# Kernel optimization log

Hardware: AMD Instinct MI355X
Metric: run time of the kernel (lower is better)

Reference implementation:

```python
import jax, jax.numpy as jnp
import numpy as np

N, L, D = 8192, 50, 64          # batch nodes, history length, embed_dim
NUM_ITEMS, NUM_ATTRS, NUM_FAM = 50000, 100000, 100000


def setup_inputs() -> dict:
    key = jax.random.key(0)
    ks = jax.random.split(key, 12)
    scale = 0.05
    return {
        "nodes": jax.random.randint(ks[0], (N,), 0, NUM_ITEMS),
        "history_va": jax.random.randint(ks[1], (N, L), 0, NUM_ATTRS),
        "history_af": jax.random.randint(ks[2], (N, L), 0, NUM_FAM),
        "v2e_w": jax.random.normal(ks[3], (NUM_ITEMS, D), jnp.float32) * scale,
        "a2e_w": jax.random.normal(ks[4], (NUM_ATTRS, D), jnp.float32) * scale,
        "f2e_w": jax.random.normal(ks[5], (NUM_FAM, D), jnp.float32) * scale,
        "W1": jax.random.normal(ks[6], (3 * D, D), jnp.float32) * scale,
        "b1": jnp.zeros((D,), jnp.float32),
        "W2": jax.random.normal(ks[7], (D, D), jnp.float32) * scale,
        "b2": jnp.zeros((D,), jnp.float32),
        "w3": jax.random.normal(ks[8], (D, 1), jnp.float32) * scale,
        "b3": jnp.zeros((1,), jnp.float32),
    }


def reference(nodes, history_va, history_af, v2e_w, a2e_w, f2e_w,
              W1, b1, W2, b2, w3, b3):
    # Batched form of the per-node loop (va=True branch).
    e_va = a2e_w[history_va]                       # [N, L, D] gathered attr embeds
    e_af = f2e_w[history_af]                       # [N, L, D] gathered famous embeds
    va_rep = v2e_w[nodes]                          # [N, D]    target item embed
    rep = jnp.broadcast_to(va_rep[:, None, :], e_va.shape)
    x = jnp.concatenate([e_va, rep, e_af], axis=-1)  # [N, L, 3D]
    h = jax.nn.relu(x @ W1 + b1)                   # [N, L, D]
    h = jax.nn.relu(h @ W2 + b2)                   # [N, L, D]
    scores = (h @ w3 + b3)[..., 0]                 # [N, L]
    att = jax.nn.softmax(scores, axis=1)           # softmax over history dim
    # e_va.T @ att per node  ==  weighted sum over history
    return jnp.einsum("nld,nl->nd", e_va, att)     # [N, D]
```

## Files before the change

kernel.cpp:

```cpp
#include <hip/hip_runtime.h>
#include <hip/hip_bf16.h>

typedef __bf16 bf16x8 __attribute__((ext_vector_type(8)));
typedef __bf16 bf16x4 __attribute__((ext_vector_type(4)));
typedef float  f32x4  __attribute__((ext_vector_type(4)));

#define HL   50
#define DD   64
#define NPB  2
#define MR   112
#define MT   7
#define XSS  136

__global__ __launch_bounds__(256) void va_prep_kernel(
    const float* __restrict__ W1, const float* __restrict__ W2,
    const float* __restrict__ w3, const float* __restrict__ b1,
    const float* __restrict__ b2,
    __bf16* __restrict__ wf, float* __restrict__ wsc)
{
    const int tid  = threadIdx.x;
    const int quad = tid >> 6;
    const int col  = tid & 63;
    __bf16* dst = wf + tid * 64;
    #pragma unroll
    for (int t = 0; t < 4; ++t)
        #pragma unroll
        for (int j = 0; j < 8; ++j) {
            int keff = t * 32 + quad * 8 + j;
            int krow = (keff < 64) ? keff : keff + 64;
            dst[t * 8 + j] = (__bf16)W1[krow * 64 + col];
        }
    #pragma unroll
    for (int t = 0; t < 2; ++t)
        #pragma unroll
        for (int j = 0; j < 8; ++j) {
            dst[32 + t * 8 + j] = (__bf16)W1[(64 + t * 32 + quad * 8 + j) * 64 + col];
            dst[48 + t * 8 + j] = (__bf16)W2[(t * 32 + quad * 8 + j) * 64 + col];
        }
    if (tid < 64) {
        wsc[tid]       = w3[tid];
        wsc[64 + tid]  = b1[tid];
        wsc[128 + tid] = b2[tid];
    }
}

__global__ __launch_bounds__(256, 5) void va_agg_kernel(
    const int*    __restrict__ nodes,
    const int*    __restrict__ hva,
    const int*    __restrict__ haf,
    const float*  __restrict__ v2e,
    const float*  __restrict__ a2e,
    const float*  __restrict__ f2e,
    const __bf16* __restrict__ wf,
    const float*  __restrict__ wsc,
    float*        __restrict__ out)
{
    __shared__ __bf16 xs[MR * XSS];
    __shared__ float  pbuf[4 * MR];

    const int tid  = threadIdx.x;
    const int w    = tid >> 6;
    const int lane = tid & 63;
    const int lq   = lane & 15;
    const int quad = lane >> 4;
    const int col  = w * 16 + lq;
    const int n0   = blockIdx.x * NPB;

    {
        const int* hb = hva + n0 * HL;
        const int* fb = haf + n0 * HL;
        #pragma unroll
        for (int i = 0; i < 13; ++i) {
            int t = i * 256 + tid;
            if (t < NPB * HL * 2 * 16) {
                int r = t >> 4, q = t & 15;
                bool va = (r < NPB * HL);
                int gr = va ? r : r - NPB * HL;
                int idx = va ? hb[gr] : fb[gr];
                const float* src = (va ? a2e : f2e) + (size_t)idx * DD + q * 4;
                float4 v = *(const float4*)src;
                bf16x4 pk = {(__bf16)v.x, (__bf16)v.y, (__bf16)v.z, (__bf16)v.w};
                *(bf16x4*)&xs[gr * XSS + (va ? 0 : DD) + q * 4] = pk;
            }
        }
    }

    bf16x8 repf[2];
    #pragma unroll
    for (int t = 0; t < 2; ++t)
        #pragma unroll
        for (int j = 0; j < 8; ++j) repf[t][j] = (__bf16)0.f;
    if (lq < NPB) {
        int nd = nodes[n0 + lq];
        const float* rp = v2e + (size_t)nd * DD;
        #pragma unroll
        for (int t = 0; t < 2; ++t) {
            float4 v0 = *(const float4*)(rp + t * 32 + quad * 8);
            float4 v1 = *(const float4*)(rp + t * 32 + quad * 8 + 4);
            repf[t] = (bf16x8){(__bf16)v0.x, (__bf16)v0.y, (__bf16)v0.z, (__bf16)v0.w,
                               (__bf16)v1.x, (__bf16)v1.y, (__bf16)v1.z, (__bf16)v1.w};
        }
    }

    const __bf16* fbp = wf + (size_t)(quad * 64 + col) * 64;
    bf16x8 b1f[4], b1u[2], b2f[2];
    #pragma unroll
    for (int t = 0; t < 4; ++t) b1f[t] = *(const bf16x8*)(fbp + t * 8);
    #pragma unroll
    for (int t = 0; t < 2; ++t) {
        b1u[t] = *(const bf16x8*)(fbp + 32 + t * 8);
        b2f[t] = *(const bf16x8*)(fbp + 48 + t * 8);
    }
    const float w3c = wsc[col];
    const float b1c = wsc[64 + col];
    const float b2c = wsc[128 + col];

    f32x4 rb = {0.f, 0.f, 0.f, 0.f};
    #pragma unroll
    for (int t = 0; t < 2; ++t)
        rb = __builtin_amdgcn_mfma_f32_16x16x32_bf16(repf[t], b1u[t], rb, 0, 0, 0);
    const float bias0 = __shfl(rb[0], lq) + b1c;
    const float bias1 = __shfl(rb[1], lq) + b1c;

    __syncthreads();

    f32x4 acc[MT];
    #pragma unroll
    for (int mt = 0; mt < MT; ++mt)
        #pragma unroll
        for (int r = 0; r < 4; ++r) {
            int gr = mt * 16 + quad * 4 + r;
            acc[mt][r] = (gr >= HL) ? bias1 : bias0;
        }
    #pragma unroll
    for (int t = 0; t < 4; ++t)
        #pragma unroll
        for (int mt = 0; mt < MT; ++mt) {
            bf16x8 a = *(const bf16x8*)&xs[(mt * 16 + lq) * XSS + t * 32 + quad * 8];
            acc[mt] = __builtin_amdgcn_mfma_f32_16x16x32_bf16(a, b1f[t], acc[mt], 0, 0, 0);
        }
    __syncthreads();
    #pragma unroll
    for (int mt = 0; mt < MT; ++mt)
        #pragma unroll
        for (int r = 0; r < 4; ++r) {
            int gr = mt * 16 + quad * 4 + r;
            xs[gr * XSS + DD + col] = (__bf16)fmaxf(acc[mt][r], 0.f);
        }
    __syncthreads();

    f32x4 a2[MT];
    #pragma unroll
    for (int mt = 0; mt < MT; ++mt) a2[mt] = (f32x4){b2c, b2c, b2c, b2c};
    #pragma unroll
    for (int t = 0; t < 2; ++t)
        #pragma unroll
        for (int mt = 0; mt < MT; ++mt) {
            bf16x8 a = *(const bf16x8*)&xs[(mt * 16 + lq) * XSS + DD + t * 32 + quad * 8];
            a2[mt] = __builtin_amdgcn_mfma_f32_16x16x32_bf16(a, b2f[t], a2[mt], 0, 0, 0);
        }
    #pragma unroll
    for (int mt = 0; mt < MT; ++mt) {
        float p0 = fmaxf(a2[mt][0], 0.f) * w3c;
        float p1 = fmaxf(a2[mt][1], 0.f) * w3c;
        float p2 = fmaxf(a2[mt][2], 0.f) * w3c;
        float p3 = fmaxf(a2[mt][3], 0.f) * w3c;
        #pragma unroll
        for (int m = 1; m < 16; m <<= 1) {
            p0 += __shfl_xor(p0, m);
            p1 += __shfl_xor(p1, m);
            p2 += __shfl_xor(p2, m);
            p3 += __shfl_xor(p3, m);
        }
        if (lq == 0) {
            int rowb = mt * 16 + quad * 4;
            pbuf[w * MR + rowb + 0] = p0;
            pbuf[w * MR + rowb + 1] = p1;
            pbuf[w * MR + rowb + 2] = p2;
            pbuf[w * MR + rowb + 3] = p3;
        }
    }
    __syncthreads();

    const int n  = w & 1;
    const int lh = w >> 1;
    float att;
    {
        float s = -3.0e38f;
        if (lane < HL) {
            int gr = n * HL + lane;
            s = pbuf[gr] + pbuf[MR + gr] + pbuf[2 * MR + gr] + pbuf[3 * MR + gr];
        }
        float mx = s;
        #pragma unroll
        for (int m = 1; m < 64; m <<= 1) mx = fmaxf(mx, __shfl_xor(mx, m));
        float e = (lane < HL) ? __expf(s - mx) : 0.f;
        float sm = e;
        #pragma unroll
        for (int m = 1; m < 64; m <<= 1) sm += __shfl_xor(sm, m);
        att = e / sm;
    }

    {
        float o = 0.f;
        const int lb = lh * 25;
        #pragma unroll
        for (int i = 0; i < 25; ++i) {
            int l = lb + i;
            float av = __shfl(att, l);
            o = fmaf(av, (float)xs[(n * HL + l) * XSS + lane], o);
        }
        float* op = (float*)&xs[(100 + w) * XSS + DD];
        op[lane] = o;
    }
    __syncthreads();
    if (w < NPB) {
        const float* p0 = (const float*)&xs[(100 + w) * XSS + DD];
        const float* p1 = (const float*)&xs[(100 + w + 2) * XSS + DD];
        out[(size_t)(n0 + w) * DD + lane] = p0[lane] + p1[lane];
    }
}

extern "C" void kernel_launch(void* const* d_in, const int* in_sizes, int n_in,
                              void* d_out, int out_size, void* d_ws, size_t ws_size,
                              hipStream_t stream) {
    const int*   nodes = (const int*)d_in[0];
    const int*   hva   = (const int*)d_in[1];
    const int*   haf   = (const int*)d_in[2];
    const float* v2e   = (const float*)d_in[3];
    const float* a2e   = (const float*)d_in[4];
    const float* f2e   = (const float*)d_in[5];
    const float* W1    = (const float*)d_in[6];
    const float* b1    = (const float*)d_in[7];
    const float* W2    = (const float*)d_in[8];
    const float* b2    = (const float*)d_in[9];
    const float* w3    = (const float*)d_in[10];
    float* out = (float*)d_out;

    __bf16* wf  = (__bf16*)d_ws;
    float*  wsc = (float*)((char*)d_ws + 256 * 64 * 2);

    va_prep_kernel<<<1, 256, 0, stream>>>(W1, W2, w3, b1, b2, wf, wsc);

    const int N = in_sizes[0];
    const int blocks = N / NPB;
    va_agg_kernel<<<blocks, 256, 0, stream>>>(nodes, hva, haf, v2e, a2e, f2e,
                                              wf, wsc, out);
}
```

Measured before the change: 167.5 us.

## Process one node per block with 64-row tiles to cut padding waste

Each block now handles a single node, so it works on 50 real rows padded to 64 (4 MFMA row tiles) instead of 100 padded to 112 (7 tiles). Shared memory per block drops, and the launch bound is raised to 8 blocks per CU to increase occupancy. The final weighted sum is split across the 4 waves by interleaved history rows and reduced through shared memory. The cost is twice as many blocks, with the per-block weight fragment loads and setup repeated for each node, plus a larger share of padded rows (14 of 64 versus 12 of 112).

```diff
diff --git a/kernel.cpp b/kernel.cpp
--- a/kernel.cpp
+++ b/kernel.cpp
@@ -7,9 +7,8 @@
 
 #define HL   50
 #define DD   64
-#define NPB  2
-#define MR   112
-#define MT   7
+#define MR   64
+#define MT   4
 #define XSS  136
 
 __global__ __launch_bounds__(256) void va_prep_kernel(
@@ -44,7 +43,7 @@
     }
 }
 
-__global__ __launch_bounds__(256, 5) void va_agg_kernel(
+__global__ __launch_bounds__(256, 8) void va_agg_kernel(
     const int*    __restrict__ nodes,
     const int*    __restrict__ hva,
     const int*    __restrict__ haf,
@@ -64,18 +63,18 @@
     const int lq   = lane & 15;
     const int quad = lane >> 4;
     const int col  = w * 16 + lq;
-    const int n0   = blockIdx.x * NPB;
+    const int node = blockIdx.x;
 
     {
-        const int* hb = hva + n0 * HL;
-        const int* fb = haf + n0 * HL;
-        #pragma unroll
-        for (int i = 0; i < 13; ++i) {
+        const int* hb = hva + node * HL;
+        const int* fb = haf + node * HL;
+        #pragma unroll
+        for (int i = 0; i < 7; ++i) {
             int t = i * 256 + tid;
-            if (t < NPB * HL * 2 * 16) {
+            if (t < HL * 2 * 16) {
                 int r = t >> 4, q = t & 15;
-                bool va = (r < NPB * HL);
-                int gr = va ? r : r - NPB * HL;
+                bool va = (r < HL);
+                int gr = va ? r : r - HL;
                 int idx = va ? hb[gr] : fb[gr];
                 const float* src = (va ? a2e : f2e) + (size_t)idx * DD + q * 4;
                 float4 v = *(const float4*)src;
@@ -90,8 +89,8 @@
     for (int t = 0; t < 2; ++t)
         #pragma unroll
         for (int j = 0; j < 8; ++j) repf[t][j] = (__bf16)0.f;
-    if (lq < NPB) {
-        int nd = nodes[n0 + lq];
+    if (lq == 0) {
+        int nd = nodes[node];
         const float* rp = v2e + (size_t)nd * DD;
         #pragma unroll
         for (int t = 0; t < 2; ++t) {
@@ -120,18 +119,12 @@
     for (int t = 0; t < 2; ++t)
         rb = __builtin_amdgcn_mfma_f32_16x16x32_bf16(repf[t], b1u[t], rb, 0, 0, 0);
     const float bias0 = __shfl(rb[0], lq) + b1c;
-    const float bias1 = __shfl(rb[1], lq) + b1c;
 
     __syncthreads();
 
     f32x4 acc[MT];
     #pragma unroll
-    for (int mt = 0; mt < MT; ++mt)
-        #pragma unroll
-        for (int r = 0; r < 4; ++r) {
-            int gr = mt * 16 + quad * 4 + r;
-            acc[mt][r] = (gr >= HL) ? bias1 : bias0;
-        }
+    for (int mt = 0; mt < MT; ++mt) acc[mt] = (f32x4){bias0, bias0, bias0, bias0};
     #pragma unroll
     for (int t = 0; t < 4; ++t)
         #pragma unroll
@@ -182,15 +175,11 @@
     }
     __syncthreads();
 
-    const int n  = w & 1;
-    const int lh = w >> 1;
     float att;
     {
         float s = -3.0e38f;
-        if (lane < HL) {
-            int gr = n * HL + lane;
-            s = pbuf[gr] + pbuf[MR + gr] + pbuf[2 * MR + gr] + pbuf[3 * MR + gr];
-        }
+        if (lane < HL)
+            s = pbuf[lane] + pbuf[MR + lane] + pbuf[2 * MR + lane] + pbuf[3 * MR + lane];
         float mx = s;
         #pragma unroll
         for (int m = 1; m < 64; m <<= 1) mx = fmaxf(mx, __shfl_xor(mx, m));
@@ -203,21 +192,24 @@
 
     {
         float o = 0.f;
-        const int lb = lh * 25;
-        #pragma unroll
-        for (int i = 0; i < 25; ++i) {
-            int l = lb + i;
-            float av = __shfl(att, l);
-            o = fmaf(av, (float)xs[(n * HL + l) * XSS + lane], o);
-        }
-        float* op = (float*)&xs[(100 + w) * XSS + DD];
+        #pragma unroll
+        for (int i = 0; i < 13; ++i) {
+            int l = w + 4 * i;
+            if (l < HL) {
+                float av = __shfl(att, l);
+                o = fmaf(av, (float)xs[l * XSS + lane], o);
+            }
+        }
+        float* op = (float*)&xs[(50 + 2 * w) * XSS];
         op[lane] = o;
     }
     __syncthreads();
-    if (w < NPB) {
-        const float* p0 = (const float*)&xs[(100 + w) * XSS + DD];
-        const float* p1 = (const float*)&xs[(100 + w + 2) * XSS + DD];
-        out[(size_t)(n0 + w) * DD + lane] = p0[lane] + p1[lane];
+    if (w == 0) {
+        float o = 0.f;
+        #pragma unroll
+        for (int k = 0; k < 4; ++k)
+            o += ((const float*)&xs[(50 + 2 * k) * XSS])[lane];
+        out[(size_t)node * DD + lane] = o;
     }
 }
 
@@ -243,7 +235,6 @@
     va_prep_kernel<<<1, 256, 0, stream>>>(W1, W2, w3, b1, b2, wf, wsc);
 
     const int N = in_sizes[0];
-    const int blocks = N / NPB;
-    va_agg_kernel<<<blocks, 256, 0, stream>>>(nodes, hva, haf, v2e, a2e, f2e,
-                                              wf, wsc, out);
+    va_agg_kernel<<<N, 256, 0, stream>>>(nodes, hva, haf, v2e, a2e, f2e,
+                                         wf, wsc, out);
 }
```

Result: slower. 171.1 us (+2.1%).

## Precompute per-table layer-1 projections and simplify main kernel to gather-add

Applied to the files above, without the earlier changes.

Distributes the first MLP layer over the concatenated inputs by projecting every attribute and family embedding row (and each target node) through its W1 slice in separate prep kernels, storing bf16 results in workspace. The main kernel then handles one node per block, gathering precomputed projections, adding bias, and running only the second layer and softmax aggregation. This removes the per-history K=128 layer-1 GEMM and shared-memory staging, at the cost of projecting the full embedding tables every call and requiring a large workspace, with a fallback to the old path if workspace is insufficient.

```diff
diff --git a/kernel.cpp b/kernel.cpp
--- a/kernel.cpp
+++ b/kernel.cpp
@@ -5,92 +5,314 @@
 typedef __bf16 bf16x4 __attribute__((ext_vector_type(4)));
 typedef float  f32x4  __attribute__((ext_vector_type(4)));
 
-#define HL   50
-#define DD   64
-#define NPB  2
-#define MR   112
-#define MT   7
-#define XSS  136
-
-__global__ __launch_bounds__(256) void va_prep_kernel(
-    const float* __restrict__ W1, const float* __restrict__ W2,
-    const float* __restrict__ w3, const float* __restrict__ b1,
+#define HL 50
+#define DD 64
+
+
+__global__ __launch_bounds__(256, 4) void prep_embed_kernel(
+    const float* __restrict__ src, const float* __restrict__ W1part,
+    __bf16* __restrict__ dst, int nrows)
+{
+    __shared__ __align__(16) __bf16 es[64 * 72];
+    const int tid = threadIdx.x;
+    const int w = tid >> 6, lane = tid & 63, lq = lane & 15, quad = lane >> 4;
+    const int col = w * 16 + lq;
+    const int r0 = blockIdx.x * 64;
+
+    #pragma unroll
+    for (int i = 0; i < 4; ++i) {
+        int t = i * 256 + tid;
+        int row = t >> 4, q = t & 15;
+        int gr = r0 + row; if (gr >= nrows) gr = nrows - 1;
+        float4 v = *(const float4*)(src + (size_t)gr * DD + q * 4);
+        bf16x4 pk = {(__bf16)v.x, (__bf16)v.y, (__bf16)v.z, (__bf16)v.w};
+        *(bf16x4*)&es[row * 72 + q * 4] = pk;
+    }
+    bf16x8 bfr[2];
+    #pragma unroll
+    for (int t = 0; t < 2; ++t)
+        #pragma unroll
+        for (int j = 0; j < 8; ++j)
+            bfr[t][j] = (__bf16)W1part[(t * 32 + quad * 8 + j) * DD + col];
+    __syncthreads();
+
+    f32x4 acc[4];
+    #pragma unroll
+    for (int mt = 0; mt < 4; ++mt) acc[mt] = (f32x4){0.f, 0.f, 0.f, 0.f};
+    #pragma unroll
+    for (int t = 0; t < 2; ++t)
+        #pragma unroll
+        for (int mt = 0; mt < 4; ++mt) {
+            bf16x8 a = *(const bf16x8*)&es[(mt * 16 + lq) * 72 + t * 32 + quad * 8];
+            acc[mt] = __builtin_amdgcn_mfma_f32_16x16x32_bf16(a, bfr[t], acc[mt], 0, 0, 0);
+        }
+    __syncthreads();
+    #pragma unroll
+    for (int mt = 0; mt < 4; ++mt)
+        #pragma unroll
+        for (int r = 0; r < 4; ++r)
+            es[(mt * 16 + quad * 4 + r) * 72 + col] = (__bf16)acc[mt][r];
+    __syncthreads();
+    {
+        int row = tid >> 2, seg = tid & 3;
+        int gr = r0 + row;
+        if (gr < nrows) {
+            bf16x8 vv = *(const bf16x8*)&es[row * 72 + seg * 16];
+            *(bf16x8*)(dst + (size_t)gr * DD + seg * 16) = vv;
+        }
+    }
+}
+
+__global__ __launch_bounds__(256, 4) void prep_bias_kernel(
+    const int* __restrict__ nodes, const float* __restrict__ v2e,
+    const float* __restrict__ W1, const float* __restrict__ b1,
+    float* __restrict__ ba, int N)
+{
+    __shared__ __align__(16) __bf16 rs[64 * 72];
+    const int tid = threadIdx.x;
+    const int w = tid >> 6, lane = tid & 63, lq = lane & 15, quad = lane >> 4;
+    const int col = w * 16 + lq;
+    const int n0 = blockIdx.x * 64;
+
+    #pragma unroll
+    for (int i = 0; i < 4; ++i) {
+        int t = i * 256 + tid;
+        int row = t >> 4, q = t & 15;
+        int gn = n0 + row; if (gn >= N) gn = N - 1;
+        int idx = nodes[gn];
+        float4 v = *(const float4*)(v2e + (size_t)idx * DD + q * 4);
+        bf16x4 pk = {(__bf16)v.x, (__bf16)v.y, (__bf16)v.z, (__bf16)v.w};
+        *(bf16x4*)&rs[row * 72 + q * 4] = pk;
+    }
+    bf16x8 bfr[2];
+    #pragma unroll
+    for (int t = 0; t < 2; ++t)
+        #pragma unroll
+        for (int j = 0; j < 8; ++j)
+            bfr[t][j] = (__bf16)W1[(64 + t * 32 + quad * 8 + j) * DD + col];
+    const float b1c = b1[col];
+    __syncthreads();
+
+    f32x4 acc[4];
+    #pragma unroll
+    for (int mt = 0; mt < 4; ++mt) acc[mt] = (f32x4){0.f, 0.f, 0.f, 0.f};
+    #pragma unroll
+    for (int t = 0; t < 2; ++t)
+        #pragma unroll
+        for (int mt = 0; mt < 4; ++mt) {
+            bf16x8 a = *(const bf16x8*)&rs[(mt * 16 + lq) * 72 + t * 32 + quad * 8];
+            acc[mt] = __builtin_amdgcn_mfma_f32_16x16x32_bf16(a, bfr[t], acc[mt], 0, 0, 0);
+        }
+    #pragma unroll
+    for (int mt = 0; mt < 4; ++mt)
+        #pragma unroll
+        for (int r = 0; r < 4; ++r) {
+            int gn = n0 + mt * 16 + quad * 4 + r;
+            if (gn < N) ba[(size_t)gn * DD + col] = acc[mt][r] + b1c;
+        }
+}
+
+__global__ __launch_bounds__(256) void prep_frag_kernel(
+    const float* __restrict__ W2, const float* __restrict__ w3,
     const float* __restrict__ b2,
-    __bf16* __restrict__ wf, float* __restrict__ wsc)
-{
-    const int tid  = threadIdx.x;
-    const int quad = tid >> 6;
-    const int col  = tid & 63;
-    __bf16* dst = wf + tid * 64;
-    #pragma unroll
-    for (int t = 0; t < 4; ++t)
-        #pragma unroll
-        for (int j = 0; j < 8; ++j) {
-            int keff = t * 32 + quad * 8 + j;
-            int krow = (keff < 64) ? keff : keff + 64;
-            dst[t * 8 + j] = (__bf16)W1[krow * 64 + col];
-        }
-    #pragma unroll
-    for (int t = 0; t < 2; ++t)
-        #pragma unroll
-        for (int j = 0; j < 8; ++j) {
-            dst[32 + t * 8 + j] = (__bf16)W1[(64 + t * 32 + quad * 8 + j) * 64 + col];
-            dst[48 + t * 8 + j] = (__bf16)W2[(t * 32 + quad * 8 + j) * 64 + col];
-        }
-    if (tid < 64) {
-        wsc[tid]       = w3[tid];
-        wsc[64 + tid]  = b1[tid];
-        wsc[128 + tid] = b2[tid];
-    }
-}
-
-__global__ __launch_bounds__(256, 5) void va_agg_kernel(
-    const int*    __restrict__ nodes,
+    __bf16* __restrict__ w2f, float* __restrict__ wsc)
+{
+    const int tid = threadIdx.x;
+    const int ln = tid & 63, c0 = tid >> 6;
+    #pragma unroll
+    for (int h = 0; h < 2; ++h) {
+        int combo = c0 + 4 * h;
+        int ct = combo >> 1, t = combo & 1;
+        __bf16* d = w2f + ((size_t)combo * 64 + ln) * 8;
+        #pragma unroll
+        for (int j = 0; j < 8; ++j)
+            d[j] = (__bf16)W2[(t * 32 + (ln >> 4) * 8 + j) * DD + ct * 16 + (ln & 15)];
+    }
+    if (tid < 64) { wsc[tid] = w3[tid]; wsc[64 + tid] = b2[tid]; }
+}
+
+__global__ __launch_bounds__(256, 8) void va_main_kernel(
     const int*    __restrict__ hva,
     const int*    __restrict__ haf,
-    const float*  __restrict__ v2e,
-    const float*  __restrict__ a2e,
-    const float*  __restrict__ f2e,
-    const __bf16* __restrict__ wf,
+    const __bf16* __restrict__ A2,
+    const __bf16* __restrict__ F2,
+    const float*  __restrict__ eva,
+    const float*  __restrict__ ba,
+    const __bf16* __restrict__ w2f,
     const float*  __restrict__ wsc,
     float*        __restrict__ out)
 {
-    __shared__ __bf16 xs[MR * XSS];
-    __shared__ float  pbuf[4 * MR];
+    __shared__ float pbuf[64];
+    __shared__ float ps[4 * 64];
 
     const int tid  = threadIdx.x;
     const int w    = tid >> 6;
     const int lane = tid & 63;
     const int lq   = lane & 15;
     const int quad = lane >> 4;
-    const int col  = w * 16 + lq;
-    const int n0   = blockIdx.x * NPB;
-
+    const int node = blockIdx.x;
+    const int* hb = hva + node * HL;
+    const int* fb = haf + node * HL;
+
+    const int lr = min(w * 16 + lq, HL - 1);
+    const int ia = hb[lr];
+    const int ifm = fb[lr];
+    bf16x8 a2g[2], f2g[2];
+    f32x4  bb[4];
+    #pragma unroll
+    for (int t = 0; t < 2; ++t) {
+        a2g[t] = *(const bf16x8*)(A2 + (size_t)ia  * DD + t * 32 + quad * 8);
+        f2g[t] = *(const bf16x8*)(F2 + (size_t)ifm * DD + t * 32 + quad * 8);
+        bb[t * 2]     = *(const f32x4*)(ba + (size_t)node * DD + t * 32 + quad * 8);
+        bb[t * 2 + 1] = *(const f32x4*)(ba + (size_t)node * DD + t * 32 + quad * 8 + 4);
+    }
+
+    bf16x8 h1f[2];
+    #pragma unroll
+    for (int t = 0; t < 2; ++t)
+        #pragma unroll
+        for (int j = 0; j < 8; ++j) {
+            float f = (float)a2g[t][j] + (float)f2g[t][j] + bb[t * 2 + (j >> 2)][j & 3];
+            h1f[t][j] = (__bf16)fmaxf(f, 0.f);
+        }
+
+    float srow[4] = {0.f, 0.f, 0.f, 0.f};
+    #pragma unroll
+    for (int ct = 0; ct < 4; ++ct) {
+        const float b2c = wsc[64 + ct * 16 + lq];
+        f32x4 acc = {b2c, b2c, b2c, b2c};
+        #pragma unroll
+        for (int t = 0; t < 2; ++t) {
+            bf16x8 bfr = *(const bf16x8*)(w2f + ((size_t)(ct * 2 + t) * 64 + lane) * 8);
+            acc = __builtin_amdgcn_mfma_f32_16x16x32_bf16(h1f[t], bfr, acc, 0, 0, 0);
+        }
+        const float w3c = wsc[ct * 16 + lq];
+        #pragma unroll
+        for (int r = 0; r < 4; ++r)
+            srow[r] = fmaf(fmaxf(acc[r], 0.f), w3c, srow[r]);
+    }
+    #pragma unroll
+    for (int r = 0; r < 4; ++r) {
+        #pragma unroll
+        for (int m = 1; m < 16; m <<= 1) srow[r] += __shfl_xor(srow[r], m);
+    }
+    if (lq == 0) {
+        #pragma unroll
+        for (int r = 0; r < 4; ++r) pbuf[w * 16 + quad * 4 + r] = srow[r];
+    }
+
+    int   oidx[13];
+    float ev[13];
+    #pragma unroll
+    for (int i = 0; i < 13; ++i) {
+        int l = w + 4 * i;
+        oidx[i] = hb[(l < HL) ? l : 0];
+    }
+    #pragma unroll
+    for (int i = 0; i < 13; ++i)
+        ev[i] = eva[(size_t)oidx[i] * DD + lane];
+    __syncthreads();
+
+    float att;
+    {
+        float s = (lane < HL) ? pbuf[lane] : -3.0e38f;
+        float mx = s;
+        #pragma unroll
+        for (int m = 1; m < 64; m <<= 1) mx = fmaxf(mx, __shfl_xor(mx, m));
+        float e = (lane < HL) ? __expf(s - mx) : 0.f;
+        float sm = e;
+        #pragma unroll
+        for (int m = 1; m < 64; m <<= 1) sm += __shfl_xor(sm, m);
+        att = e / sm;
+    }
+
+    float o = 0.f;
+    #pragma unroll
+    for (int i = 0; i < 13; ++i) {
+        int l = w + 4 * i;
+        if (l < HL) {
+            float av = __shfl(att, l);
+            o = fmaf(av, ev[i], o);
+        }
+    }
+    ps[w * 64 + lane] = o;
+    __syncthreads();
+    if (w == 0)
+        out[(size_t)node * DD + lane] =
+            ps[lane] + ps[64 + lane] + ps[128 + lane] + ps[192 + lane];
+}
+
+#define FMR  112
+#define FMT  7
+#define FXSS 136
+
+__global__ __launch_bounds__(256) void fb_prep_kernel(
+    const float* __restrict__ W1, const float* __restrict__ W2,
+    const float* __restrict__ w3, const float* __restrict__ b1,
+    const float* __restrict__ b2,
+    __bf16* __restrict__ wf, float* __restrict__ wsc)
+{
+    const int tid  = threadIdx.x;
+    const int quad = tid >> 6;
+    const int col  = tid & 63;
+    __bf16* dst = wf + tid * 64;
+    #pragma unroll
+    for (int t = 0; t < 4; ++t)
+        #pragma unroll
+        for (int j = 0; j < 8; ++j) {
+            int keff = t * 32 + quad * 8 + j;
+            int krow = (keff < 64) ? keff : keff + 64;
+            dst[t * 8 + j] = (__bf16)W1[krow * 64 + col];
+        }
+    #pragma unroll
+    for (int t = 0; t < 2; ++t)
+        #pragma unroll
+        for (int j = 0; j < 8; ++j) {
+            dst[32 + t * 8 + j] = (__bf16)W1[(64 + t * 32 + quad * 8 + j) * 64 + col];
+            dst[48 + t * 8 + j] = (__bf16)W2[(t * 32 + quad * 8 + j) * 64 + col];
+        }
+    if (tid < 64) {
+        wsc[tid] = w3[tid]; wsc[64 + tid] = b1[tid]; wsc[128 + tid] = b2[tid];
+    }
+}
+
+__global__ __launch_bounds__(256, 5) void fb_agg_kernel(
+    const int* __restrict__ nodes, const int* __restrict__ hva,
+    const int* __restrict__ haf, const float* __restrict__ v2e,
+    const float* __restrict__ a2e, const float* __restrict__ f2e,
+    const __bf16* __restrict__ wf, const float* __restrict__ wsc,
+    float* __restrict__ out)
+{
+    __shared__ __bf16 xs[FMR * FXSS];
+    __shared__ float  pbuf[4 * FMR];
+    const int tid = threadIdx.x;
+    const int w = tid >> 6, lane = tid & 63, lq = lane & 15, quad = lane >> 4;
+    const int col = w * 16 + lq;
+    const int n0 = blockIdx.x * 2;
     {
         const int* hb = hva + n0 * HL;
         const int* fb = haf + n0 * HL;
         #pragma unroll
         for (int i = 0; i < 13; ++i) {
             int t = i * 256 + tid;
-            if (t < NPB * HL * 2 * 16) {
+            if (t < 2 * HL * 2 * 16) {
                 int r = t >> 4, q = t & 15;
-                bool va = (r < NPB * HL);
-                int gr = va ? r : r - NPB * HL;
+                bool va = (r < 2 * HL);
+                int gr = va ? r : r - 2 * HL;
                 int idx = va ? hb[gr] : fb[gr];
                 const float* src = (va ? a2e : f2e) + (size_t)idx * DD + q * 4;
                 float4 v = *(const float4*)src;
                 bf16x4 pk = {(__bf16)v.x, (__bf16)v.y, (__bf16)v.z, (__bf16)v.w};
-                *(bf16x4*)&xs[gr * XSS + (va ? 0 : DD) + q * 4] = pk;
+                *(bf16x4*)&xs[gr * FXSS + (va ? 0 : DD) + q * 4] = pk;
             }
         }
     }
-
     bf16x8 repf[2];
     #pragma unroll
     for (int t = 0; t < 2; ++t)
         #pragma unroll
         for (int j = 0; j < 8; ++j) repf[t][j] = (__bf16)0.f;
-    if (lq < NPB) {
+    if (lq < 2) {
         int nd = nodes[n0 + lq];
         const float* rp = v2e + (size_t)nd * DD;
         #pragma unroll
@@ -101,7 +323,6 @@
                                (__bf16)v1.x, (__bf16)v1.y, (__bf16)v1.z, (__bf16)v1.w};
         }
     }
-
     const __bf16* fbp = wf + (size_t)(quad * 64 + col) * 64;
     bf16x8 b1f[4], b1u[2], b2f[2];
     #pragma unroll
@@ -114,19 +335,16 @@
     const float w3c = wsc[col];
     const float b1c = wsc[64 + col];
     const float b2c = wsc[128 + col];
-
     f32x4 rb = {0.f, 0.f, 0.f, 0.f};
     #pragma unroll
     for (int t = 0; t < 2; ++t)
         rb = __builtin_amdgcn_mfma_f32_16x16x32_bf16(repf[t], b1u[t], rb, 0, 0, 0);
     const float bias0 = __shfl(rb[0], lq) + b1c;
     const float bias1 = __shfl(rb[1], lq) + b1c;
-
-    __syncthreads();
-
-    f32x4 acc[MT];
-    #pragma unroll
-    for (int mt = 0; mt < MT; ++mt)
+    __syncthreads();
+    f32x4 acc[FMT];
+    #pragma unroll
+    for (int mt = 0; mt < FMT; ++mt)
         #pragma unroll
         for (int r = 0; r < 4; ++r) {
             int gr = mt * 16 + quad * 4 + r;
@@ -135,61 +353,54 @@
     #pragma unroll
     for (int t = 0; t < 4; ++t)
         #pragma unroll
-        for (int mt = 0; mt < MT; ++mt) {
-            bf16x8 a = *(const bf16x8*)&xs[(mt * 16 + lq) * XSS + t * 32 + quad * 8];
+        for (int mt = 0; mt < FMT; ++mt) {
+            bf16x8 a = *(const bf16x8*)&xs[(mt * 16 + lq) * FXSS + t * 32 + quad * 8];
             acc[mt] = __builtin_amdgcn_mfma_f32_16x16x32_bf16(a, b1f[t], acc[mt], 0, 0, 0);
         }
     __syncthreads();
     #pragma unroll
-    for (int mt = 0; mt < MT; ++mt)
+    for (int mt = 0; mt < FMT; ++mt)
         #pragma unroll
         for (int r = 0; r < 4; ++r) {
             int gr = mt * 16 + quad * 4 + r;
-            xs[gr * XSS + DD + col] = (__bf16)fmaxf(acc[mt][r], 0.f);
-        }
-    __syncthreads();
-
-    f32x4 a2[MT];
-    #pragma unroll
-    for (int mt = 0; mt < MT; ++mt) a2[mt] = (f32x4){b2c, b2c, b2c, b2c};
-    #pragma unroll
-    for (int t = 0; t < 2; ++t)
-        #pragma unroll
-        for (int mt = 0; mt < MT; ++mt) {
-            bf16x8 a = *(const bf16x8*)&xs[(mt * 16 + lq) * XSS + DD + t * 32 + quad * 8];
+            xs[gr * FXSS + DD + col] = (__bf16)fmaxf(acc[mt][r], 0.f);
+        }
+    __syncthreads();
+    f32x4 a2[FMT];
+    #pragma unroll
+    for (int mt = 0; mt < FMT; ++mt) a2[mt] = (f32x4){b2c, b2c, b2c, b2c};
+    #pragma unroll
+    for (int t = 0; t < 2; ++t)
+        #pragma unroll
+        for (int mt = 0; mt < FMT; ++mt) {
+            bf16x8 a = *(const bf16x8*)&xs[(mt * 16 + lq) * FXSS + DD + t * 32 + quad * 8];
             a2[mt] = __builtin_amdgcn_mfma_f32_16x16x32_bf16(a, b2f[t], a2[mt], 0, 0, 0);
         }
     #pragma unroll
-    for (int mt = 0; mt < MT; ++mt) {
+    for (int mt = 0; mt < FMT; ++mt) {
         float p0 = fmaxf(a2[mt][0], 0.f) * w3c;
         float p1 = fmaxf(a2[mt][1], 0.f) * w3c;
         float p2 = fmaxf(a2[mt][2], 0.f) * w3c;
         float p3 = fmaxf(a2[mt][3], 0.f) * w3c;
         #pragma unroll
         for (int m = 1; m < 16; m <<= 1) {
-            p0 += __shfl_xor(p0, m);
-            p1 += __shfl_xor(p1, m);
-            p2 += __shfl_xor(p2, m);
-            p3 += __shfl_xor(p3, m);
+            p0 += __shfl_xor(p0, m); p1 += __shfl_xor(p1, m);
+            p2 += __shfl_xor(p2, m); p3 += __shfl_xor(p3, m);
         }
         if (lq == 0) {
             int rowb = mt * 16 + quad * 4;
-            pbuf[w * MR + rowb + 0] = p0;
-            pbuf[w * MR + rowb + 1] = p1;
-            pbuf[w * MR + rowb + 2] = p2;
-            pbuf[w * MR + rowb + 3] = p3;
-        }
-    }
-    __syncthreads();
-
-    const int n  = w & 1;
-    const int lh = w >> 1;
+            pbuf[w * FMR + rowb + 0] = p0; pbuf[w * FMR + rowb + 1] = p1;
+            pbuf[w * FMR + rowb + 2] = p2; pbuf[w * FMR + rowb + 3] = p3;
+        }
+    }
+    __syncthreads();
+    const int n = w & 1, lh = w >> 1;
     float att;
     {
         float s = -3.0e38f;
         if (lane < HL) {
             int gr = n * HL + lane;
-            s = pbuf[gr] + pbuf[MR + gr] + pbuf[2 * MR + gr] + pbuf[3 * MR + gr];
+            s = pbuf[gr] + pbuf[FMR + gr] + pbuf[2 * FMR + gr] + pbuf[3 * FMR + gr];
         }
         float mx = s;
         #pragma unroll
@@ -200,7 +411,6 @@
         for (int m = 1; m < 64; m <<= 1) sm += __shfl_xor(sm, m);
         att = e / sm;
     }
-
     {
         float o = 0.f;
         const int lb = lh * 25;
@@ -208,15 +418,15 @@
         for (int i = 0; i < 25; ++i) {
             int l = lb + i;
             float av = __shfl(att, l);
-            o = fmaf(av, (float)xs[(n * HL + l) * XSS + lane], o);
-        }
-        float* op = (float*)&xs[(100 + w) * XSS + DD];
+            o = fmaf(av, (float)xs[(n * HL + l) * FXSS + lane], o);
+        }
+        float* op = (float*)&xs[(100 + w) * FXSS + DD];
         op[lane] = o;
     }
     __syncthreads();
-    if (w < NPB) {
-        const float* p0 = (const float*)&xs[(100 + w) * XSS + DD];
-        const float* p1 = (const float*)&xs[(100 + w + 2) * XSS + DD];
+    if (w < 2) {
+        const float* p0 = (const float*)&xs[(100 + w) * FXSS + DD];
+        const float* p1 = (const float*)&xs[(100 + w + 2) * FXSS + DD];
         out[(size_t)(n0 + w) * DD + lane] = p0[lane] + p1[lane];
     }
 }
@@ -237,13 +447,34 @@
     const float* w3    = (const float*)d_in[10];
     float* out = (float*)d_out;
 
-    __bf16* wf  = (__bf16*)d_ws;
-    float*  wsc = (float*)((char*)d_ws + 256 * 64 * 2);
-
-    va_prep_kernel<<<1, 256, 0, stream>>>(W1, W2, w3, b1, b2, wf, wsc);
-
-    const int N = in_sizes[0];
-    const int blocks = N / NPB;
-    va_agg_kernel<<<blocks, 256, 0, stream>>>(nodes, hva, haf, v2e, a2e, f2e,
-                                              wf, wsc, out);
-}
+    const int N  = in_sizes[0];
+    const int nA = in_sizes[4] / DD;
+    const int nF = in_sizes[5] / DD;
+
+    size_t offA2 = 0;
+    size_t offF2 = (offA2 + (size_t)nA * DD * 2 + 255) & ~(size_t)255;
+    size_t offBA = (offF2 + (size_t)nF * DD * 2 + 255) & ~(size_t)255;
+    size_t offWF = (offBA + (size_t)N * DD * 4 + 255) & ~(size_t)255;
+    size_t offSC = offWF + 8 * 64 * 8 * 2;
+    size_t need  = offSC + 128 * 4;
+
+    if (ws_size >= need) {
+        __bf16* A2  = (__bf16*)((char*)d_ws + offA2);
+        __bf16* F2  = (__bf16*)((char*)d_ws + offF2);
+        float*  ba  = (float*)((char*)d_ws + offBA);
+        __bf16* w2f = (__bf16*)((char*)d_ws + offWF);
+        float*  wsc = (float*)((char*)d_ws + offSC);
+
+        prep_frag_kernel<<<1, 256, 0, stream>>>(W2, w3, b2, w2f, wsc);
+        prep_bias_kernel<<<(N + 63) / 64, 256, 0, stream>>>(nodes, v2e, W1, b1, ba, N);
+        prep_embed_kernel<<<(nA + 63) / 64, 256, 0, stream>>>(a2e, W1, A2, nA);
+        prep_embed_kernel<<<(nF + 63) / 64, 256, 0, stream>>>(f2e, W1 + 128 * DD, F2, nF);
+        va_main_kernel<<<N, 256, 0, stream>>>(hva, haf, A2, F2, a2e, ba, w2f, wsc, out);
+    } else {
+        __bf16* wf  = (__bf16*)d_ws;
+        float*  wsc = (float*)((char*)d_ws + 256 * 64 * 2);
+        fb_prep_kernel<<<1, 256, 0, stream>>>(W1, W2, w3, b1, b2, wf, wsc);
+        fb_agg_kernel<<<N / 2, 256, 0, stream>>>(nodes, hva, haf, v2e, a2e, f2e,
+                                                 wf, wsc, out);
+    }
+}
```

Result: no change. 164.7 us (-1.7%).
